# Optimization experiments

Hardware: AMD Instinct MI355X
Metric: run time of the kernel (lower is better)

Reference implementation:

```python
import jax, jax.numpy as jnp
import numpy as np

LATENT, U_DIM, NUM_PROD, NUM_INJ, FEAT_C = 128, 30, 20, 10, 128
WELL_IN = LATENT + U_DIM + FEAT_C  # 286
HID = 64
B = 16384


def setup_inputs() -> dict:
    key = jax.random.key(0)
    ks = jax.random.split(key, 12)
    s = lambda fan_in: 1.0 / np.sqrt(fan_in)
    return {
        "zt": jax.random.normal(ks[0], (B, LATENT), jnp.float32),
        "dt": 1,
        "ut": jax.random.normal(ks[1], (B, U_DIM), jnp.float32),
        "well_features": jax.random.normal(ks[2], (B, NUM_PROD, FEAT_C), jnp.float32),
        # StructuredODEFunc params: dz/dt = -(L L^T) z + Bm u
        "L": jax.random.normal(ks[3], (LATENT, LATENT), jnp.float32) * s(LATENT),
        "Bm": jax.random.normal(ks[4], (LATENT, U_DIM), jnp.float32) * s(U_DIM),
        # per-well MLP heads, stacked: [P, in, out]
        "W1": jax.random.uniform(ks[5], (NUM_PROD, WELL_IN, HID), jnp.float32, -s(WELL_IN), s(WELL_IN)),
        "b1": jax.random.uniform(ks[6], (NUM_PROD, HID), jnp.float32, -s(WELL_IN), s(WELL_IN)),
        "W2": jax.random.uniform(ks[7], (NUM_PROD, HID, 2), jnp.float32, -s(HID), s(HID)),
        "b2": jax.random.uniform(ks[8], (NUM_PROD, 2), jnp.float32, -s(HID), s(HID)),
        # injector head: Linear(latent+u_dim, num_inj)
        "Wi": jax.random.uniform(ks[9], (LATENT + U_DIM, NUM_INJ), jnp.float32, -s(LATENT + U_DIM), s(LATENT + U_DIM)),
        "bi": jax.random.uniform(ks[10], (NUM_INJ,), jnp.float32, -s(LATENT + U_DIM), s(LATENT + U_DIM)),
    }


def reference(zt, dt, ut, well_features, L, Bm, W1, b1, W2, b2, Wi, bi):
    # ODE step: A = -L L^T, f(z) = A z + Bm u; euler over t_span [0,1] -> one step h=1
    A = -(L @ L.T)                                  # [D, D]
    zt1 = zt + zt @ A.T + ut @ Bm.T                 # [B, D]
    zu = jnp.concatenate([zt1, ut], axis=-1)        # [B, D+U]
    # per-well heads, fused as batched gather-MLP
    zu_b = jnp.broadcast_to(zu[:, None, :], (zu.shape[0], NUM_PROD, zu.shape[1]))
    head_in = jnp.concatenate([zu_b, well_features], axis=-1)        # [B, P, WELL_IN]
    h = jax.nn.relu(jnp.einsum('bpi,pih->bph', head_in, W1) + b1)    # [B, P, 64]
    well_out = jnp.einsum('bph,pho->bpo', h, W2) + b2                # [B, P, 2]
    well_out = well_out.reshape(well_out.shape[0], NUM_PROD * 2)     # concat order matches loop
    inj_out = zu @ Wi + bi                                           # [B, num_inj]
    yt1 = jnp.concatenate([well_out, inj_out], axis=-1)              # [B, 2P+I]
    return zt1, yt1
```

## Files before the change

### kernel.cpp

```cpp
#include <hip/hip_runtime.h>

#define BATCH   16384
#define LATENT  128
#define U_DIM   30
#define NUM_PROD 20
#define NUM_INJ 10
#define FEAT_C  128
#define WELL_IN 286
#define HID     64
#define ZT1_N   (BATCH*LATENT)
#define OUT_ROW (NUM_PROD*2+NUM_INJ)

typedef unsigned short u16;
typedef __attribute__((ext_vector_type(8))) short  short8;
typedef __attribute__((ext_vector_type(4))) float  floatx4;

__device__ __forceinline__ u16 f2bf(float f){
    unsigned x = __builtin_bit_cast(unsigned, f);
    x += 0x7fffu + ((x >> 16) & 1u);
    return (u16)(x >> 16);
}
__device__ __forceinline__ short8 cvt8(floatx4 a, floatx4 b){
    short8 s;
    s[0]=(short)f2bf(a[0]); s[1]=(short)f2bf(a[1]);
    s[2]=(short)f2bf(a[2]); s[3]=(short)f2bf(a[3]);
    s[4]=(short)f2bf(b[0]); s[5]=(short)f2bf(b[1]);
    s[6]=(short)f2bf(b[2]); s[7]=(short)f2bf(b[3]);
    return s;
}

#define NW1  368640
#define NGS  20480
#define NWIS 2560
#define NW2S 20480
__device__ u16 g_w1s[NW1];
__device__ u16 g_gs [NGS];
__device__ u16 g_wis[NWIS];
__device__ u16 g_w2s[NW2S];

__global__ __launch_bounds__(256) void prep_kernel(
    const float* __restrict__ L, const float* __restrict__ Bm,
    const float* __restrict__ W1, const float* __restrict__ Wi,
    const float* __restrict__ W2)
{
    const int bx = blockIdx.x, t = threadIdx.x;
    if (bx < 180) {
        int s = bx*256 + t;
        int lane = s & 63;
        int rest = s >> 6;
        int kk = rest % 9, pn = rest / 9;
        int n0 = pn & 3, p = pn >> 2;
        int kbase = kk*32 + ((lane>>4)*8);
        int n = n0*16 + (lane & 15);
        short8 v;
#pragma unroll
        for (int j = 0; j < 8; j++) {
            int k = kbase + j;
            u16 b = 0;
            if (k < 158)        b = f2bf(W1[(p*WELL_IN + k)*HID + n]);
            else if (k >= 160)  b = f2bf(W1[(p*WELL_IN + (k-2))*HID + n]);
            v[j] = (short)b;
        }
        *(short8*)&g_w1s[(size_t)s*8] = v;
        return;
    }
    if (bx < 272) {
        int sid = (bx-180)*256 + t;
        if (sid < NW2S) {
            int j=sid&7, lane=(sid>>3)&63, rest=sid>>9;
            int kk=rest&1, p=rest>>1;
            int k=kk*32+((lane>>4)*8)+j, n=lane&15;
            g_w2s[sid] = (n<2) ? f2bf(W2[(p*HID+k)*2+n]) : (u16)0;
            return;
        }
        sid -= NW2S;
        if (sid < NWIS) {
            int j=sid&7, lane=(sid>>3)&63, kk=sid>>9;
            int k=kk*32+((lane>>4)*8)+j, n=lane&15;
            g_wis[sid] = (k<158 && n<NUM_INJ) ? f2bf(Wi[k*NUM_INJ+n]) : (u16)0;
            return;
        }
        sid -= NWIS;
        if (sid < 512) {
            int lane=sid&63, nt=sid>>6;
            int q=lane>>4, n=nt*16+(lane&15);
#pragma unroll
            for (int j = 0; j < 8; j++) {
                int u = q*8 + j;
                float v = (u < U_DIM) ? Bm[n*U_DIM + u] : 0.f;
                g_gs[((nt*5+4)*64 + lane)*8 + j] = f2bf(v);
            }
        }
        return;
    }
    const int mt = bx - 272;
    const int w = t>>6, lane=t&63, q=lane>>4, m=lane&15;
    floatx4 accG[2];
    accG[0]=(floatx4){0.f,0.f,0.f,0.f}; accG[1]=(floatx4){0.f,0.f,0.f,0.f};
#pragma unroll
    for (int kk = 0; kk < 4; kk++) {
        const float* ap = &L[(mt*16+m)*128 + kk*32 + q*8];
        short8 a = cvt8(*(const floatx4*)ap, *(const floatx4*)(ap+4));
#pragma unroll
        for (int ntl = 0; ntl < 2; ntl++) {
            int nt = w*2 + ntl;
            const float* bp = &L[(nt*16+m)*128 + kk*32 + q*8];
            short8 b = cvt8(*(const floatx4*)bp, *(const floatx4*)(bp+4));
            accG[ntl] = __builtin_amdgcn_mfma_f32_16x16x32_bf16(a, b, accG[ntl], 0, 0, 0);
        }
    }
#pragma unroll
    for (int ntl = 0; ntl < 2; ntl++)
#pragma unroll
        for (int r = 0; r < 4; r++) {
            int kg = mt*16 + q*4 + r;
            int n  = (w*2+ntl)*16 + m;
            float v = ((kg==n) ? 1.f : 0.f) - accG[ntl][r];
            int fi = ((n>>4)*5 + (kg>>5))*512 + (((kg>>3)&3)*16 + (n&15))*8 + (kg&7);
            g_gs[fi] = f2bf(v);
        }
}

__global__ __launch_bounds__(256) __attribute__((amdgpu_waves_per_eu(2,2)))
void ker_main(
    const float* __restrict__ zt, const float* __restrict__ ut,
    const float* __restrict__ wff, const float* __restrict__ b1,
    const float* __restrict__ b2,  const float* __restrict__ bi,
    const float* __restrict__ W2g,
    float* __restrict__ outf)
{
    __shared__ alignas(16) u16   zus[32][168];
    __shared__ alignas(16) u16   wfb[4096];
    __shared__ alignas(16) u16   w1l[18432];
    __shared__ alignas(16) float outs[32][50];
    __shared__ alignas(16) float w2l[2560];
    __shared__ alignas(16) float b1l[1280];
    const int t = threadIdx.x;
    const int row0 = blockIdx.x * 32;
    const int w = t >> 6, lane = t & 63, q = lane >> 4, m = lane & 15;

    const int lane_s = t & 63, cs = (t >> 6) & 3;
    const int qs = lane_s >> 4, ms = lane_s & 15;

    floatx4 fr[4];
    auto issue = [&](int p){
#pragma unroll
        for (int rt = 0; rt < 2; rt++) {
            const float* pb = &wff[((size_t)(row0 + rt*16 + ms)*NUM_PROD + p)*FEAT_C + cs*32 + qs*8];
            fr[rt*2+0] = *(const floatx4*)pb;
            fr[rt*2+1] = *(const floatx4*)(pb + 4);
        }
    };
    issue(0);

    for (int i = t; i < 1024; i += 256) {
        int r = i >> 5, c4 = i & 31;
        floatx4 v = *(const floatx4*)&zt[(size_t)(row0 + r)*128 + c4*4];
        u16* d = &zus[r][c4*4];
        d[0]=f2bf(v[0]); d[1]=f2bf(v[1]); d[2]=f2bf(v[2]); d[3]=f2bf(v[3]);
    }
    for (int i = t; i < 960; i += 256) {
        int r = i / U_DIM, c = i - r*U_DIM;
        zus[r][128 + c] = f2bf(ut[(row0 + r)*U_DIM + c]);
    }
    if (t < 64) zus[t >> 1][158 + (t & 1)] = 0;
    for (int i = t; i < 2560; i += 256) w2l[i] = W2g[i];
    for (int i = t; i < 1280; i += 256) b1l[i] = b1[i];
    for (int i = t; i < 1600; i += 256) {
        int col = i % 50;
        (&outs[0][0])[i] = (col < 40) ? b2[col] : 0.f;
    }
    __syncthreads();

    {
        const int mt = w & 1, ng = (w >> 1) * 4;
        floatx4 acc[4];
#pragma unroll
        for (int c = 0; c < 4; c++) acc[c] = (floatx4){0.f,0.f,0.f,0.f};
#pragma unroll
        for (int kk = 0; kk < 5; kk++) {
            short8 a = *(const short8*)&zus[mt*16 + m][kk*32 + q*8];
#pragma unroll
            for (int c = 0; c < 4; c++) {
                short8 b = *(const short8*)&g_gs[(((ng+c)*5 + kk)*64 + lane)*8];
                acc[c] = __builtin_amdgcn_mfma_f32_16x16x32_bf16(a, b, acc[c], 0, 0, 0);
            }
        }
        __syncthreads();
#pragma unroll
        for (int c = 0; c < 4; c++)
#pragma unroll
            for (int r = 0; r < 4; r++) {
                int row = mt*16 + q*4 + r;
                int col = (ng+c)*16 + m;
                float v = acc[c][r];
                outf[(size_t)(row0 + row)*128 + col] = v;
                zus[row][col] = f2bf(v);
            }
    }
    __syncthreads();

    short8 za0[5], za1[5];
#pragma unroll
    for (int kk = 0; kk < 5; kk++) {
        za0[kk] = *(const short8*)&zus[m][kk*32 + q*8];
        za1[kk] = *(const short8*)&zus[16 + m][kk*32 + q*8];
    }

    if (w == 3) {
        floatx4 ai[2];
        ai[0]=(floatx4){0.f,0.f,0.f,0.f}; ai[1]=(floatx4){0.f,0.f,0.f,0.f};
#pragma unroll
        for (int kk = 0; kk < 5; kk++) {
            short8 b = *(const short8*)&g_wis[(kk*64 + lane)*8];
            ai[0] = __builtin_amdgcn_mfma_f32_16x16x32_bf16(za0[kk], b, ai[0], 0, 0, 0);
            ai[1] = __builtin_amdgcn_mfma_f32_16x16x32_bf16(za1[kk], b, ai[1], 0, 0, 0);
        }
        if (m < NUM_INJ) {
            float bv = bi[m];
#pragma unroll
            for (int rt = 0; rt < 2; rt++)
#pragma unroll
                for (int r = 0; r < 4; r++)
                    outs[rt*16 + q*4 + r][40 + m] = ai[rt][r] + bv;
        }
    }

    for (int p = 0; p < NUM_PROD; p++) {
        short8 wv[9];
#pragma unroll
        for (int i = 0; i < 9; i++) {
            int f = (t >> 6) + i*4;
            wv[i] = *(const short8*)&g_w1s[(((size_t)p*36 + f)*64 + lane_s)*8];
        }
        *(short8*)&wfb[((0*4 + cs)*64 + lane_s)*8] = cvt8(fr[0], fr[1]);
        *(short8*)&wfb[((1*4 + cs)*64 + lane_s)*8] = cvt8(fr[2], fr[3]);
#pragma unroll
        for (int i = 0; i < 9; i++) {
            int f = (t >> 6) + i*4;
            *(short8*)&w1l[(size_t)(f*64 + lane_s)*8] = wv[i];
        }
        __syncthreads();
        if (p + 1 < NUM_PROD) issue(p + 1);

        short8 bq[9];
#pragma unroll
        for (int kk = 0; kk < 9; kk++)
            bq[kk] = *(const short8*)&w1l[((w*9 + kk)*64 + lane)*8];
        short8 wa[2][4];
#pragma unroll
        for (int rt = 0; rt < 2; rt++)
#pragma unroll
            for (int kk = 0; kk < 4; kk++)
                wa[rt][kk] = *(const short8*)&wfb[((rt*4 + kk)*64 + lane)*8];
        floatx4 h0 = (floatx4){0.f,0.f,0.f,0.f};
        floatx4 h1 = (floatx4){0.f,0.f,0.f,0.f};
#pragma unroll
        for (int kk = 0; kk < 9; kk++) {
            short8 a0 = (kk < 5) ? za0[kk] : wa[0][kk-5];
            short8 a1 = (kk < 5) ? za1[kk] : wa[1][kk-5];
            h0 = __builtin_amdgcn_mfma_f32_16x16x32_bf16(a0, bq[kk], h0, 0, 0, 0);
            h1 = __builtin_amdgcn_mfma_f32_16x16x32_bf16(a1, bq[kk], h1, 0, 0, 0);
        }
        const int col = w*16 + m;
        const float bb  = b1l[p*64 + col];
        const float w2x = w2l[(p*64 + col)*2 + 0];
        const float w2y = w2l[(p*64 + col)*2 + 1];
#pragma unroll
        for (int rt = 0; rt < 2; rt++) {
            floatx4 hv = rt ? h1 : h0;
            float s[8];
#pragma unroll
            for (int r = 0; r < 4; r++) {
                float h = hv[r] + bb;
                h = h > 0.f ? h : 0.f;
                s[r*2+0] = h * w2x;
                s[r*2+1] = h * w2y;
            }
#pragma unroll
            for (int mask = 1; mask < 16; mask <<= 1)
#pragma unroll
                for (int i = 0; i < 8; i++)
                    s[i] += __shfl_xor(s[i], mask);
            float val = (m==0)?s[0]:(m==1)?s[1]:(m==2)?s[2]:(m==3)?s[3]
                       :(m==4)?s[4]:(m==5)?s[5]:(m==6)?s[6]:s[7];
            if (m < 8)
                atomicAdd(&outs[rt*16 + q*4 + (m>>1)][p*2 + (m&1)], val);
        }
        __syncthreads();
    }

    {
        const float* of = &outs[0][0];
        float* dst = outf + (size_t)ZT1_N + (size_t)row0 * OUT_ROW;
        for (int i = t; i < 400; i += 256)
            *(floatx4*)&dst[i*4] = *(const floatx4*)&of[i*4];
    }
}

extern "C" void kernel_launch(void* const* d_in, const int* in_sizes, int n_in,
                              void* d_out, int out_size, void* d_ws, size_t ws_size,
                              hipStream_t stream)
{
    const float* zt = (const float*)d_in[0];
    const float* ut = (const float*)d_in[2];
    const float* wf = (const float*)d_in[3];
    const float* L  = (const float*)d_in[4];
    const float* Bm = (const float*)d_in[5];
    const float* W1 = (const float*)d_in[6];
    const float* b1 = (const float*)d_in[7];
    const float* W2 = (const float*)d_in[8];
    const float* b2 = (const float*)d_in[9];
    const float* Wi = (const float*)d_in[10];
    const float* bi = (const float*)d_in[11];
    float* outf = (float*)d_out;

    prep_kernel<<<280, 256, 0, stream>>>(L, Bm, W1, Wi, W2);
    ker_main<<<BATCH/32, 256, 0, stream>>>(zt, ut, wf, b1, b2, bi, W2, outf);
}
```

Before: 293.0 us.

## Process two wells per iteration with register-prefetched W1 fragments

```diff
diff --git a/kernel.cpp b/kernel.cpp
--- a/kernel.cpp
+++ b/kernel.cpp
@@ -130,8 +130,8 @@
     float* __restrict__ outf)
 {
     __shared__ alignas(16) u16   zus[32][168];
-    __shared__ alignas(16) u16   wfb[4096];
-    __shared__ alignas(16) u16   w1l[18432];
+    __shared__ alignas(16) u16   wfb0[4096];
+    __shared__ alignas(16) u16   wfb1[4096];
     __shared__ alignas(16) float outs[32][50];
     __shared__ alignas(16) float w2l[2560];
     __shared__ alignas(16) float b1l[1280];
@@ -142,16 +142,22 @@
     const int lane_s = t & 63, cs = (t >> 6) & 3;
     const int qs = lane_s >> 4, ms = lane_s & 15;
 
-    floatx4 fr[4];
-    auto issue = [&](int p){
+    floatx4 rA[4], rB[4];
+    auto issue = [&](floatx4 (&r)[4], int p){
 #pragma unroll
         for (int rt = 0; rt < 2; rt++) {
             const float* pb = &wff[((size_t)(row0 + rt*16 + ms)*NUM_PROD + p)*FEAT_C + cs*32 + qs*8];
-            fr[rt*2+0] = *(const floatx4*)pb;
-            fr[rt*2+1] = *(const floatx4*)(pb + 4);
+            r[rt*2+0] = *(const floatx4*)pb;
+            r[rt*2+1] = *(const floatx4*)(pb + 4);
         }
     };
-    issue(0);
+    auto cstore = [&](const floatx4 (&r)[4], u16* __restrict__ wfb){
+        *(short8*)&wfb[((0*4 + cs)*64 + lane_s)*8] = cvt8(r[0], r[1]);
+        *(short8*)&wfb[((1*4 + cs)*64 + lane_s)*8] = cvt8(r[2], r[3]);
+    };
+
+    issue(rA, 0);
+    issue(rB, 1);
 
     for (int i = t; i < 1024; i += 256) {
         int r = i >> 5, c4 = i & 31;
@@ -200,21 +206,17 @@
     }
     __syncthreads();
 
-    short8 za0[5], za1[5];
-#pragma unroll
-    for (int kk = 0; kk < 5; kk++) {
-        za0[kk] = *(const short8*)&zus[m][kk*32 + q*8];
-        za1[kk] = *(const short8*)&zus[16 + m][kk*32 + q*8];
-    }
-
     if (w == 3) {
         floatx4 ai[2];
         ai[0]=(floatx4){0.f,0.f,0.f,0.f}; ai[1]=(floatx4){0.f,0.f,0.f,0.f};
 #pragma unroll
         for (int kk = 0; kk < 5; kk++) {
             short8 b = *(const short8*)&g_wis[(kk*64 + lane)*8];
-            ai[0] = __builtin_amdgcn_mfma_f32_16x16x32_bf16(za0[kk], b, ai[0], 0, 0, 0);
-            ai[1] = __builtin_amdgcn_mfma_f32_16x16x32_bf16(za1[kk], b, ai[1], 0, 0, 0);
+#pragma unroll
+            for (int rt = 0; rt < 2; rt++) {
+                short8 a = *(const short8*)&zus[rt*16 + m][kk*32 + q*8];
+                ai[rt] = __builtin_amdgcn_mfma_f32_16x16x32_bf16(a, b, ai[rt], 0, 0, 0);
+            }
         }
         if (m < NUM_INJ) {
             float bv = bi[m];
@@ -226,41 +228,29 @@
         }
     }
 
-    for (int p = 0; p < NUM_PROD; p++) {
-        short8 wv[9];
-#pragma unroll
-        for (int i = 0; i < 9; i++) {
-            int f = (t >> 6) + i*4;
-            wv[i] = *(const short8*)&g_w1s[(((size_t)p*36 + f)*64 + lane_s)*8];
-        }
-        *(short8*)&wfb[((0*4 + cs)*64 + lane_s)*8] = cvt8(fr[0], fr[1]);
-        *(short8*)&wfb[((1*4 + cs)*64 + lane_s)*8] = cvt8(fr[2], fr[3]);
-#pragma unroll
-        for (int i = 0; i < 9; i++) {
-            int f = (t >> 6) + i*4;
-            *(short8*)&w1l[(size_t)(f*64 + lane_s)*8] = wv[i];
-        }
-        __syncthreads();
-        if (p + 1 < NUM_PROD) issue(p + 1);
-
-        short8 bq[9];
+    short8 bfrA[9], bfrB[9];
+    auto loadB = [&](short8 (&bfr)[9], int p){
 #pragma unroll
         for (int kk = 0; kk < 9; kk++)
-            bq[kk] = *(const short8*)&w1l[((w*9 + kk)*64 + lane)*8];
-        short8 wa[2][4];
-#pragma unroll
-        for (int rt = 0; rt < 2; rt++)
-#pragma unroll
-            for (int kk = 0; kk < 4; kk++)
-                wa[rt][kk] = *(const short8*)&wfb[((rt*4 + kk)*64 + lane)*8];
+            bfr[kk] = *(const short8*)&g_w1s[(((size_t)p*36 + w*9 + kk)*64 + lane)*8];
+    };
+    loadB(bfrA, 0);
+
+    auto do_well = [&](int p, const u16* __restrict__ wfb, const short8 (&bfr)[9]){
         floatx4 h0 = (floatx4){0.f,0.f,0.f,0.f};
         floatx4 h1 = (floatx4){0.f,0.f,0.f,0.f};
 #pragma unroll
         for (int kk = 0; kk < 9; kk++) {
-            short8 a0 = (kk < 5) ? za0[kk] : wa[0][kk-5];
-            short8 a1 = (kk < 5) ? za1[kk] : wa[1][kk-5];
-            h0 = __builtin_amdgcn_mfma_f32_16x16x32_bf16(a0, bq[kk], h0, 0, 0, 0);
-            h1 = __builtin_amdgcn_mfma_f32_16x16x32_bf16(a1, bq[kk], h1, 0, 0, 0);
+            short8 a0, a1;
+            if (kk < 5) {
+                a0 = *(const short8*)&zus[m][kk*32 + q*8];
+                a1 = *(const short8*)&zus[16 + m][kk*32 + q*8];
+            } else {
+                a0 = *(const short8*)&wfb[((0*4 + kk-5)*64 + lane)*8];
+                a1 = *(const short8*)&wfb[((1*4 + kk-5)*64 + lane)*8];
+            }
+            h0 = __builtin_amdgcn_mfma_f32_16x16x32_bf16(a0, bfr[kk], h0, 0, 0, 0);
+            h1 = __builtin_amdgcn_mfma_f32_16x16x32_bf16(a1, bfr[kk], h1, 0, 0, 0);
         }
         const int col = w*16 + m;
         const float bb  = b1l[p*64 + col];
@@ -287,6 +277,18 @@
             if (m < 8)
                 atomicAdd(&outs[rt*16 + q*4 + (m>>1)][p*2 + (m&1)], val);
         }
+    };
+
+    for (int tb = 0; tb < 20; tb += 2) {
+        cstore(rA, wfb0);
+        cstore(rB, wfb1);
+        __syncthreads();
+        if (tb + 2 < 20) issue(rA, tb + 2);
+        if (tb + 3 < 20) issue(rB, tb + 3);
+        loadB(bfrB, tb + 1);
+        do_well(tb, wfb0, bfrA);
+        if (tb + 2 < 20) loadB(bfrA, tb + 2);
+        do_well(tb + 1, wfb1, bfrB);
         __syncthreads();
     }
 
```

New measurement: 299.4 us. 2.2% more time.
